# Optimization experiments

Hardware: AMD Instinct MI355X
Metric: run time of the kernel (lower is better)

The kernel has to match this reference:

```python
import jax, jax.numpy as jnp
import numpy as np

B, H, E, V, K = 1024, 128, 16, 100000, 512

def setup_inputs() -> dict:
    key = jax.random.key(0)
    k1, k2, k3, k4, k5 = jax.random.split(key, 5)
    return {
        "h": jax.random.normal(k1, (B, H), dtype=jnp.float32),
        "valid_indices": jax.random.randint(k2, (B, K), 0, V, dtype=jnp.int32),
        "word_embeddings": jax.random.normal(k3, (V, E), dtype=jnp.float32),
        "W": jax.random.normal(k4, (E, H), dtype=jnp.float32) * (1.0 / np.sqrt(H)),
        "b": jax.random.normal(k5, (E,), dtype=jnp.float32) * 0.01,
    }

def reference(h, valid_indices, word_embeddings, W, b):
    # linear projection: [B,H] @ [H,E] + [E] -> [B,E]
    query = h @ W.T + b
    # scores: [B,E] @ [E,V] -> [B,V]
    scores = jnp.einsum('be,ve->bv', query, word_embeddings)
    # boolean valid mask via one batched scatter (replaces per-row python loop)
    rows = jnp.arange(B, dtype=jnp.int32)[:, None]              # [B,1]
    valid = jnp.zeros((B, V), dtype=bool).at[rows, valid_indices].set(True)
    # invalid positions get -inf added (equivalent to scores + where(mask,-inf,0))
    return jnp.where(valid, scores, -jnp.inf)
```

## Files before the change

kernel.cpp:

```cpp
#include <hip/hip_runtime.h>
#include <math.h>

#define PB 1024
#define PH 128
#define PE 16
#define PV 100000
#define PK 512

#define MASKED_HALF  ((unsigned short)0xFBFFu)
#define MASKED_PAIR  (0xFBFFFBFFu)

static constexpr int MASK_WORDS = (PV + 31) / 32;

union Pack8 {
    uint4 u4;
    unsigned short s[8];
};

__global__ __launch_bounds__(256) void PolicyHead_68685116998378_kernel(
    const float* __restrict__ h,
    const int*   __restrict__ valid_idx,
    const float* __restrict__ emb,
    const float* __restrict__ W,
    const float* __restrict__ bias,
    unsigned short* __restrict__ out)
{
    __shared__ unsigned int mask[MASK_WORDS];
    __shared__ float partials[256];
    __shared__ float query[PE];

    const int b = blockIdx.x;
    const int t = threadIdx.x;

    for (int i = t; i < MASK_WORDS; i += 256) mask[i] = 0u;

    {
        const int e = t & 15;
        const int j = t >> 4;
        const float* hrow = h + b * PH + j * 8;
        const float* wrow = W + e * PH + j * 8;
        float s = 0.f;
        #pragma unroll
        for (int i = 0; i < 8; ++i) s += hrow[i] * wrow[i];
        partials[t] = s;
    }
    __syncthreads();

    for (int k = t; k < PK; k += 256) {
        unsigned int idx = (unsigned int)valid_idx[b * PK + k];
        if (idx < PV)
            atomicOr(&mask[idx >> 5], 1u << (idx & 31));
    }
    if (t < PE) {
        float s = bias[t];
        #pragma unroll
        for (int j = 0; j < 16; ++j) s += partials[j * 16 + t];
        query[t] = s;
    }
    __syncthreads();

    float q[PE];
    #pragma unroll
    for (int i = 0; i < PE; ++i) q[i] = query[i];

    unsigned short* orow = out + (size_t)b * PV;
    const int n8 = PV / 8;
    for (int c = t; c < n8; c += 256) {
        const int v = c * 8;
        const unsigned int bits = (mask[v >> 5] >> (v & 31)) & 0xFFu;
        Pack8 r;
        r.u4 = make_uint4(MASKED_PAIR, MASKED_PAIR, MASKED_PAIR, MASKED_PAIR);
        if (bits) {
            #pragma unroll
            for (int u = 0; u < 8; ++u) {
                if (bits & (1u << u)) {
                    const float* erow = emb + (size_t)(v + u) * PE;
                    float s = 0.f;
                    #pragma unroll
                    for (int i = 0; i < PE; ++i) s += q[i] * erow[i];
                    s = (fabsf(s) < 1e30f) ? s : 0.0f;
                    unsigned int fb = __builtin_bit_cast(unsigned int, s);
                    fb += 0x7FFFu + ((fb >> 16) & 1u);
                    r.s[u] = (unsigned short)(fb >> 16);
                }
            }
        }
        *(uint4*)(orow + v) = r.u4;
    }
}

extern "C" void kernel_launch(void* const* d_in, const int* in_sizes, int n_in,
                              void* d_out, int out_size, void* d_ws, size_t ws_size,
                              hipStream_t stream) {
    const float* h    = (const float*)d_in[0];
    const int*   vi   = (const int*)  d_in[1];
    const float* emb  = (const float*)d_in[2];
    const float* W    = (const float*)d_in[3];
    const float* bias = (const float*)d_in[4];
    unsigned short* out = (unsigned short*)d_out;

    PolicyHead_68685116998378_kernel<<<dim3(PB), dim3(256), 0, stream>>>(
        h, vi, emb, W, bias, out);
}
```

Baseline: 427.3 us.

## Replace shared-memory bitmask scan with masked fill then direct scatter

Drops the per-block shared-memory validity bitmask, its clearing and its atomics. Each output row is first filled with the masked constant using vector stores. After a block barrier, each valid index computes its dot product and scatters a single bf16 value into the row. This removes the LDS footprint, which should help occupancy, and removes the divergent per-chunk bit tests. In exchange it adds scattered 2-byte global writes and relies on the barrier to order the fill stores before the scatter stores.

```diff
diff --git a/kernel.cpp b/kernel.cpp
--- a/kernel.cpp
+++ b/kernel.cpp
@@ -7,15 +7,7 @@
 #define PV 100000
 #define PK 512
 
-#define MASKED_HALF  ((unsigned short)0xFBFFu)
 #define MASKED_PAIR  (0xFBFFFBFFu)
-
-static constexpr int MASK_WORDS = (PV + 31) / 32;
-
-union Pack8 {
-    uint4 u4;
-    unsigned short s[8];
-};
 
 __global__ __launch_bounds__(256) void PolicyHead_68685116998378_kernel(
     const float* __restrict__ h,
@@ -25,14 +17,11 @@
     const float* __restrict__ bias,
     unsigned short* __restrict__ out)
 {
-    __shared__ unsigned int mask[MASK_WORDS];
     __shared__ float partials[256];
     __shared__ float query[PE];
 
     const int b = blockIdx.x;
     const int t = threadIdx.x;
-
-    for (int i = t; i < MASK_WORDS; i += 256) mask[i] = 0u;
 
     {
         const int e = t & 15;
@@ -45,12 +34,6 @@
         partials[t] = s;
     }
     __syncthreads();
-
-    for (int k = t; k < PK; k += 256) {
-        unsigned int idx = (unsigned int)valid_idx[b * PK + k];
-        if (idx < PV)
-            atomicOr(&mask[idx >> 5], 1u << (idx & 31));
-    }
     if (t < PE) {
         float s = bias[t];
         #pragma unroll
@@ -59,33 +42,32 @@
     }
     __syncthreads();
 
+    unsigned short* orow = out + (size_t)b * PV;
+    const uint4 m4 = make_uint4(MASKED_PAIR, MASKED_PAIR, MASKED_PAIR, MASKED_PAIR);
+    const int n8 = PV / 8;
+    #pragma unroll 4
+    for (int c = t; c < n8; c += 256) {
+        *(uint4*)(orow + c * 8) = m4;
+    }
+
+    __syncthreads();
+
     float q[PE];
     #pragma unroll
     for (int i = 0; i < PE; ++i) q[i] = query[i];
 
-    unsigned short* orow = out + (size_t)b * PV;
-    const int n8 = PV / 8;
-    for (int c = t; c < n8; c += 256) {
-        const int v = c * 8;
-        const unsigned int bits = (mask[v >> 5] >> (v & 31)) & 0xFFu;
-        Pack8 r;
-        r.u4 = make_uint4(MASKED_PAIR, MASKED_PAIR, MASKED_PAIR, MASKED_PAIR);
-        if (bits) {
+    for (int k = t; k < PK; k += 256) {
+        unsigned int idx = (unsigned int)valid_idx[b * PK + k];
+        if (idx < PV) {
+            const float* erow = emb + (size_t)idx * PE;
+            float s = 0.f;
             #pragma unroll
-            for (int u = 0; u < 8; ++u) {
-                if (bits & (1u << u)) {
-                    const float* erow = emb + (size_t)(v + u) * PE;
-                    float s = 0.f;
-                    #pragma unroll
-                    for (int i = 0; i < PE; ++i) s += q[i] * erow[i];
-                    s = (fabsf(s) < 1e30f) ? s : 0.0f;
-                    unsigned int fb = __builtin_bit_cast(unsigned int, s);
-                    fb += 0x7FFFu + ((fb >> 16) & 1u);
-                    r.s[u] = (unsigned short)(fb >> 16);
-                }
-            }
+            for (int i = 0; i < PE; ++i) s += q[i] * erow[i];
+            s = (fabsf(s) < 1e30f) ? s : 0.0f;
+            unsigned int fb = __builtin_bit_cast(unsigned int, s);
+            fb += 0x7FFFu + ((fb >> 16) & 1u);
+            orow[idx] = (unsigned short)(fb >> 16);
         }
-        *(uint4*)(orow + v) = r.u4;
     }
 }
 
```

Result: faster. 412.1 us (-3.6%).

## Compute scores once per valid index via popcount-prefix ranking in shared memory

Applied to the files above, without the earlier changes.

Builds a per-word popcount prefix over the valid-bit mask using a wave scan. Each valid index's bf16 score is then computed once in a dense loop over the K indices and stored by rank in a compact shared array. The output write loop looks scores up by rank instead of doing divergent dot products inline. This adds a prefix pass, extra barriers and more shared memory, which may lower occupancy.

```diff
diff --git a/kernel.cpp b/kernel.cpp
--- a/kernel.cpp
+++ b/kernel.cpp
@@ -7,10 +7,10 @@
 #define PV 100000
 #define PK 512
 
-#define MASKED_HALF  ((unsigned short)0xFBFFu)
 #define MASKED_PAIR  (0xFBFFFBFFu)
 
 static constexpr int MASK_WORDS = (PV + 31) / 32;
+static constexpr int CHUNK      = (MASK_WORDS + 255) / 256;
 
 union Pack8 {
     uint4 u4;
@@ -25,15 +25,17 @@
     const float* __restrict__ bias,
     unsigned short* __restrict__ out)
 {
-    __shared__ unsigned int mask[MASK_WORDS];
+    __shared__ unsigned int   mask[MASK_WORDS];
+    __shared__ unsigned short prefix[MASK_WORDS];
+    __shared__ unsigned short scorev[PK];
     __shared__ float partials[256];
     __shared__ float query[PE];
+    __shared__ unsigned int wavesum[4];
 
     const int b = blockIdx.x;
     const int t = threadIdx.x;
 
     for (int i = t; i < MASK_WORDS; i += 256) mask[i] = 0u;
-
     {
         const int e = t & 15;
         const int j = t >> 4;
@@ -48,8 +50,7 @@
 
     for (int k = t; k < PK; k += 256) {
         unsigned int idx = (unsigned int)valid_idx[b * PK + k];
-        if (idx < PV)
-            atomicOr(&mask[idx >> 5], 1u << (idx & 31));
+        if (idx < PV) atomicOr(&mask[idx >> 5], 1u << (idx & 31));
     }
     if (t < PE) {
         float s = bias[t];
@@ -59,29 +60,64 @@
     }
     __syncthreads();
 
+    const int cs = t * CHUNK;
+    const int ce = (cs + CHUNK < MASK_WORDS) ? cs + CHUNK : MASK_WORDS;
+    unsigned int csum = 0;
+    for (int j = cs; j < ce; ++j) csum += __popc(mask[j]);
+    unsigned int x = csum;
+    #pragma unroll
+    for (int d = 1; d < 64; d <<= 1) {
+        unsigned int y = __shfl_up(x, d, 64);
+        if ((t & 63) >= d) x += y;
+    }
+    if ((t & 63) == 63) wavesum[t >> 6] = x;
+    __syncthreads();
+    unsigned int waveoff = 0;
+    for (int w = 0; w < (t >> 6); ++w) waveoff += wavesum[w];
+    unsigned int run = waveoff + x - csum;
+    for (int j = cs; j < ce; ++j) {
+        prefix[j] = (unsigned short)run;
+        run += __popc(mask[j]);
+    }
+    __syncthreads();
+
     float q[PE];
     #pragma unroll
     for (int i = 0; i < PE; ++i) q[i] = query[i];
+
+    for (int k = t; k < PK; k += 256) {
+        unsigned int idx = (unsigned int)valid_idx[b * PK + k];
+        if (idx < PV) {
+            const unsigned int w = mask[idx >> 5];
+            const unsigned int rank =
+                prefix[idx >> 5] + __popc(w & ((1u << (idx & 31)) - 1u));
+            const float* erow = emb + (size_t)idx * PE;
+            float s = 0.f;
+            #pragma unroll
+            for (int i = 0; i < PE; ++i) s += q[i] * erow[i];
+            s = (fabsf(s) < 1e30f) ? s : 0.0f;
+            unsigned int fb = __builtin_bit_cast(unsigned int, s);
+            fb += 0x7FFFu + ((fb >> 16) & 1u);
+            scorev[rank] = (unsigned short)(fb >> 16);
+        }
+    }
+    __syncthreads();
 
     unsigned short* orow = out + (size_t)b * PV;
     const int n8 = PV / 8;
     for (int c = t; c < n8; c += 256) {
         const int v = c * 8;
-        const unsigned int bits = (mask[v >> 5] >> (v & 31)) & 0xFFu;
+        const unsigned int word = mask[v >> 5];
+        const unsigned int bits = (word >> (v & 31)) & 0xFFu;
         Pack8 r;
         r.u4 = make_uint4(MASKED_PAIR, MASKED_PAIR, MASKED_PAIR, MASKED_PAIR);
         if (bits) {
+            const unsigned int base =
+                prefix[v >> 5] + __popc(word & ((1u << (v & 31)) - 1u));
             #pragma unroll
             for (int u = 0; u < 8; ++u) {
                 if (bits & (1u << u)) {
-                    const float* erow = emb + (size_t)(v + u) * PE;
-                    float s = 0.f;
-                    #pragma unroll
-                    for (int i = 0; i < PE; ++i) s += q[i] * erow[i];
-                    s = (fabsf(s) < 1e30f) ? s : 0.0f;
-                    unsigned int fb = __builtin_bit_cast(unsigned int, s);
-                    fb += 0x7FFFu + ((fb >> 16) & 1u);
-                    r.s[u] = (unsigned short)(fb >> 16);
+                    r.s[u] = scorev[base + __popc(bits & ((1u << u) - 1u))];
                 }
             }
         }
```

Measured after the change: 383.0 us. 10.4% less time.
